# Kernel optimization log

Hardware: AMD Instinct MI355X
Metric: run time of the kernel (lower is better)

## Reference

```python
import jax, jax.numpy as jnp
import numpy as np

N_TOKEN = 267735
D = 512           # d_embed == d_proj
DIV = 4
CUTS = [0, 20000, 40000, 200000, 267735]  # cutoff_ends
N_TOKENS_BATCH = 1024  # len*bsz


def setup_inputs() -> dict:
    key = jax.random.key(0)
    ks = jax.random.split(key, 16)
    inp = {}
    inp["hidden"] = jax.random.normal(ks[0], (N_TOKENS_BATCH, D), jnp.float32)
    inp["target"] = jax.random.randint(ks[1], (N_TOKENS_BATCH,), 0, N_TOKEN)
    d_embs = [D // DIV ** i for i in range(4)]          # 512, 128, 32, 8
    sizes = [CUTS[i + 1] - CUTS[i] for i in range(4)]   # 20000, 20000, 160000, 67735
    for i in range(4):
        inp[f"W{i}"] = jax.random.normal(ks[2 + 3 * i], (sizes[i], d_embs[i]), jnp.float32) * (d_embs[i] ** -0.5)
        inp[f"b{i}"] = jax.random.normal(ks[3 + 3 * i], (sizes[i],), jnp.float32) * 0.01
        inp[f"proj{i}"] = jax.random.normal(ks[4 + 3 * i], (D, d_embs[i]), jnp.float32) * (D ** -0.5)
    inp["cluster_weight"] = jax.random.normal(ks[14], (3, D), jnp.float32) * (D ** -0.5)
    inp["cluster_bias"] = jax.random.normal(ks[15], (3,), jnp.float32) * 0.01
    return inp


def reference(hidden, target, W0, b0, proj0, W1, b1, proj1, W2, b2, proj2, W3, b3, proj3, cluster_weight, cluster_bias):
    n = jnp.arange(target.shape[0])
    # head = shortlist vocab + one logit per tail cluster
    head_w = jnp.concatenate([W0, cluster_weight], axis=0)   # [20003, D]
    head_b = jnp.concatenate([b0, cluster_bias], axis=0)     # [20003]
    head_logit = (hidden @ proj0) @ head_w.T + head_b        # einsum('bd,de,ev->bv')
    head_lp = jax.nn.log_softmax(head_logit, axis=-1)        # [N, 20003]
    head_size = head_lp.shape[1]
    # cluster id per token (0 = shortlist, 1..3 = tails)
    cid = ((target >= CUTS[1]).astype(jnp.int32)
           + (target >= CUTS[2]).astype(jnp.int32)
           + (target >= CUTS[3]).astype(jnp.int32))
    # shortlist: nll = -head_logprob[n, target]
    nll = -head_lp[n, jnp.clip(target, 0, CUTS[1] - 1)]
    for i, (Wi, bi, pi) in enumerate([(W1, b1, proj1), (W2, b2, proj2), (W3, b3, proj3)], start=1):
        l, r = CUTS[i], CUTS[i + 1]
        tail_lp = jax.nn.log_softmax((hidden @ pi) @ Wi.T + bi, axis=-1)  # [N, r-l]
        rel = jnp.clip(target - l, 0, r - l - 1)
        # faithful to original: head column indexed as head_logprob[:, -i]
        lp_i = head_lp[:, head_size - i] + tail_lp[n, rel]
        nll = jnp.where(cid == i, -lp_i, nll)
    return nll
```

## Files before the change

### kernel.cpp

```cpp
#include <hip/hip_runtime.h>

typedef short s16x8 __attribute__((ext_vector_type(8)));
typedef unsigned short u16x8 __attribute__((ext_vector_type(8)));
typedef float f32x4 __attribute__((ext_vector_type(4)));
typedef unsigned short ushort;

#define NTOK 1024
#define DHID 512

#define VH   20003
#define KH   512
#define NCH_H 80
#define TPC_H 16
#define VH_PAD 20480

#define V1   20000
#define K1   128
#define NCH_1 80
#define TPC_1 16
#define V1_PAD 20480

#define V2   160000
#define K2   32
#define NCH_2 128
#define TPC_2 80
#define V2_PAD 163840

#define V3   67735
#define K3   32
#define NCH_3 67
#define TPC_3 64
#define V3_PAD 68608

#define PAD_BIAS (-1e30f)

#define OFF_HW   0UL
#define OFF_W1   (OFF_HW  + (unsigned long)VH_PAD*KH*2)
#define OFF_W2   (OFF_W1  + (unsigned long)V1_PAD*K1*2)
#define OFF_W3   (OFF_W2  + (unsigned long)V2_PAD*K2*2)
#define OFF_HID  (OFF_W3  + (unsigned long)V3_PAD*K3*2)
#define OFF_PT0  (OFF_HID + (unsigned long)NTOK*DHID*2)
#define OFF_PT1  (OFF_PT0 + (unsigned long)512*DHID*2)
#define OFF_PT2  (OFF_PT1 + (unsigned long)128*DHID*2)
#define OFF_PT3  (OFF_PT2 + (unsigned long)32*DHID*2)
#define OFF_H0   (OFF_PT3 + (unsigned long)32*DHID*2)
#define OFF_H1   (OFF_H0  + (unsigned long)NTOK*512*2)
#define OFF_H2   (OFF_H1  + (unsigned long)NTOK*128*2)
#define OFF_H3   (OFF_H2  + (unsigned long)NTOK*32*2)
#define OFF_HB   (OFF_H3  + (unsigned long)NTOK*32*2)
#define OFF_B1   (OFF_HB  + (unsigned long)VH_PAD*4)
#define OFF_B2   (OFF_B1  + (unsigned long)V1_PAD*4)
#define OFF_B3   (OFF_B2  + (unsigned long)V2_PAD*4)
#define OFF_SH   (OFF_B3  + (unsigned long)V3_PAD*4)
#define OFF_S1   (OFF_SH  + (unsigned long)NTOK*NCH_H*4)
#define OFF_S2   (OFF_S1  + (unsigned long)NTOK*NCH_1*4)
#define OFF_S3   (OFF_S2  + (unsigned long)NTOK*NCH_2*4)

__device__ __forceinline__ ushort f2bf(float f) {
    union { float f; unsigned u; } x; x.f = f;
    unsigned r = x.u + 0x7fffu + ((x.u >> 16) & 1u);
    return (ushort)(r >> 16);
}
__device__ __forceinline__ float bf2f(ushort h) {
    union { unsigned u; float f; } x; x.u = ((unsigned)h) << 16;
    return x.f;
}
__device__ __forceinline__ f32x4 mfma_bf16(s16x8 a, s16x8 b, f32x4 c) {
    return __builtin_amdgcn_mfma_f32_16x16x32_bf16(a, b, c, 0, 0, 0);
}
__device__ __forceinline__ void ld8(const float* p, float* v) {
    float4 a = *(const float4*)p, b = *(const float4*)(p + 4);
    v[0]=a.x; v[1]=a.y; v[2]=a.z; v[3]=a.w; v[4]=b.x; v[5]=b.y; v[6]=b.z; v[7]=b.w;
}

#define WB_HW  20480L
#define WB_W1  5120L
#define WB_W2  10240L
#define WB_W3  4288L
#define WB_HID 1024L
#define WB_PT0 512L
#define WB_PT1 128L
#define WB_PT2 32L
#define WB_PT3 32L
#define WB_TOTAL (WB_HW+WB_W1+WB_W2+WB_W3+WB_HID+WB_PT0+WB_PT1+WB_PT2+WB_PT3)

__global__ __launch_bounds__(256) void prep_wswz(
    const float* __restrict__ hidden,
    const float* __restrict__ W0, const float* __restrict__ cw,
    const float* __restrict__ W1, const float* __restrict__ W2, const float* __restrict__ W3,
    const float* __restrict__ p0, const float* __restrict__ p1,
    const float* __restrict__ p2, const float* __restrict__ p3,
    ushort* __restrict__ hw, ushort* __restrict__ ow1,
    ushort* __restrict__ ow2, ushort* __restrict__ ow3,
    ushort* __restrict__ hid,
    ushort* __restrict__ pT0, ushort* __restrict__ pT1,
    ushort* __restrict__ pT2, ushort* __restrict__ pT3)
{
    int lane = threadIdx.x & 63;
    int r = lane & 15, quad = lane >> 4;
    long wb0 = (long)blockIdx.x * 4 + (threadIdx.x >> 6);
    long nw = (long)gridDim.x * 4;
    for (long wb = wb0; wb < WB_TOTAL; wb += nw) {
        long b = wb;
        float vals[8];
        #pragma unroll
        for (int j = 0; j < 8; ++j) vals[j] = 0.f;
        ushort* dst;
        if (b < WB_HW) {
            long tile = b >> 4, ks = b & 15;
            long v = tile * 16 + r, k = ks * 32 + quad * 8;
            if (v < 20000)      ld8(W0 + v * 512 + k, vals);
            else if (v < VH)    ld8(cw + (v - 20000) * 512 + k, vals);
            dst = hw + b * 512 + (long)lane * 8;
        } else if ((b -= WB_HW) < WB_W1) {
            long tile = b >> 2, ks = b & 3;
            long v = tile * 16 + r, k = ks * 32 + quad * 8;
            if (v < V1) ld8(W1 + v * 128 + k, vals);
            dst = ow1 + b * 512 + (long)lane * 8;
        } else if ((b -= WB_W1) < WB_W2) {
            long v = b * 16 + r;
            if (v < V2) ld8(W2 + v * 32 + quad * 8, vals);
            dst = ow2 + b * 512 + (long)lane * 8;
        } else if ((b -= WB_W2) < WB_W3) {
            long v = b * 16 + r;
            if (v < V3 && quad == 0) ld8(W3 + v * 8, vals);
            dst = ow3 + b * 512 + (long)lane * 8;
        } else if ((b -= WB_W3) < WB_HID) {
            long tile = b >> 4, ks = b & 15;
            long v = tile * 16 + r, k = ks * 32 + quad * 8;
            ld8(hidden + v * 512 + k, vals);
            dst = hid + b * 512 + (long)lane * 8;
        } else if ((b -= WB_HID) < WB_PT0) {
            long tile = b >> 4, ks = b & 15;
            long c = tile * 16 + r, k = ks * 32 + quad * 8;
            #pragma unroll
            for (int j = 0; j < 8; ++j) vals[j] = p0[(k + j) * 512 + c];
            dst = pT0 + b * 512 + (long)lane * 8;
        } else if ((b -= WB_PT0) < WB_PT1) {
            long tile = b >> 4, ks = b & 15;
            long c = tile * 16 + r, k = ks * 32 + quad * 8;
            #pragma unroll
            for (int j = 0; j < 8; ++j) vals[j] = p1[(k + j) * 128 + c];
            dst = pT1 + b * 512 + (long)lane * 8;
        } else if ((b -= WB_PT1) < WB_PT2) {
            long tile = b >> 4, ks = b & 15;
            long c = tile * 16 + r, k = ks * 32 + quad * 8;
            #pragma unroll
            for (int j = 0; j < 8; ++j) vals[j] = p2[(k + j) * 32 + c];
            dst = pT2 + b * 512 + (long)lane * 8;
        } else {
            b -= WB_PT2;
            long tile = b >> 4, ks = b & 15;
            long c = tile * 16 + r, k = ks * 32 + quad * 8;
            if (c < 8) {
                #pragma unroll
                for (int j = 0; j < 8; ++j) vals[j] = p3[(k + j) * 8 + c];
            }
            dst = pT3 + b * 512 + (long)lane * 8;
        }
        u16x8 o;
        #pragma unroll
        for (int j = 0; j < 8; ++j) o[j] = f2bf(vals[j]);
        *(u16x8*)dst = o;
    }
}

#define E_HB  ((long)VH_PAD)
#define E_B1  ((long)V1_PAD)
#define E_B2  ((long)V2_PAD)
#define E_B3  ((long)V3_PAD)
#define E_BIAS (E_HB+E_B1+E_B2+E_B3)

__global__ __launch_bounds__(256) void prep_bias(
    const float* __restrict__ b0, const float* __restrict__ b1,
    const float* __restrict__ b2, const float* __restrict__ b3,
    const float* __restrict__ cb,
    float* __restrict__ hbp, float* __restrict__ ob1,
    float* __restrict__ ob2, float* __restrict__ ob3)
{
    long stride = (long)gridDim.x * blockDim.x;
    for (long i = (long)blockIdx.x * blockDim.x + threadIdx.x; i < E_BIAS; i += stride) {
        long j = i;
        if (j < E_HB) {
            hbp[j] = (j < 20000) ? b0[j] : (j < VH) ? cb[j - 20000] : PAD_BIAS;
        } else if ((j -= E_HB) < E_B1) {
            ob1[j] = (j < V1) ? b1[j] : PAD_BIAS;
        } else if ((j -= E_B1) < E_B2) {
            ob2[j] = (j < V2) ? b2[j] : PAD_BIAS;
        } else { j -= E_B2;
            ob3[j] = (j < V3) ? b3[j] : PAD_BIAS;
        }
    }
}

__global__ __launch_bounds__(256) void gemm_h(
    const ushort* __restrict__ A, const ushort* __restrict__ Bt,
    ushort* __restrict__ Hout, int dpad)
{
    int wave = threadIdx.x >> 6, lane = threadIdx.x & 63;
    int quad = lane >> 4, colid = lane & 15;
    int m_tile = blockIdx.x * 4 + wave;
    int c_tile = blockIdx.y;
    const ushort* Ab = A + ((long)m_tile * 16) * 512 + lane * 8;
    const ushort* Bb = Bt + ((long)c_tile * 16) * 512 + lane * 8;
    f32x4 acc = {0.f, 0.f, 0.f, 0.f};
    #pragma unroll
    for (int ks = 0; ks < 16; ++ks) {
        s16x8 a = *(const s16x8*)(Ab + ks * 512);
        s16x8 b = *(const s16x8*)(Bb + ks * 512);
        acc = mfma_bf16(a, b, acc);
    }
    int KBo = dpad >> 5;
    int col = c_tile * 16 + colid;
    int ks_o = col >> 5, q_o = (col >> 3) & 3, j_o = col & 7;
    #pragma unroll
    for (int r = 0; r < 4; ++r) {
        int rm = quad * 4 + r;
        Hout[((long)m_tile * KBo + ks_o) * 512 + (q_o * 16 + rm) * 8 + j_o] = f2bf(acc[r]);
    }
}

template<int K, int U>
__global__ __launch_bounds__(256, 4) void fused_lse_t(
    const ushort* __restrict__ A, const ushort* __restrict__ W,
    const float* __restrict__ bias, float* __restrict__ part_s,
    int tpc, int n_chunks)
{
    constexpr int KB = K / 32;
    int wave = threadIdx.x >> 6, lane = threadIdx.x & 63;
    int quad = lane >> 4, colid = lane & 15;
    int m_tile = blockIdx.x * 4 + wave;
    int t0 = blockIdx.y * tpc;
    const ushort* Ab = A + ((long)m_tile * KB) * 512 + lane * 8;
    float s_acc[4] = {0.f, 0.f, 0.f, 0.f};

    for (int vt = 0; vt < tpc; vt += U) {
        int tile0 = t0 + vt;
        const ushort* Wb = W + ((long)tile0 * KB) * 512 + lane * 8;
        f32x4 acc[U];
        #pragma unroll
        for (int u = 0; u < U; ++u) acc[u] = (f32x4){0.f, 0.f, 0.f, 0.f};
        #pragma unroll 4
        for (int ks = 0; ks < KB; ++ks) {
            s16x8 a = *(const s16x8*)(Ab + ks * 512);
            #pragma unroll
            for (int u = 0; u < U; ++u) {
                s16x8 b = *(const s16x8*)(Wb + ((long)u * KB + ks) * 512);
                acc[u] = mfma_bf16(a, b, acc[u]);
            }
        }
        #pragma unroll
        for (int u = 0; u < U; ++u) {
            float bval = bias[(tile0 + u) * 16 + colid];
            #pragma unroll
            for (int r = 0; r < 4; ++r)
                s_acc[r] += __expf(acc[u][r] + bval);
        }
    }
    #pragma unroll
    for (int r = 0; r < 4; ++r) {
        float v = s_acc[r];
        v += __shfl_xor(v, 1);
        v += __shfl_xor(v, 2);
        v += __shfl_xor(v, 4);
        v += __shfl_xor(v, 8);
        s_acc[r] = v;
    }
    if (colid == 0) {
        #pragma unroll
        for (int r = 0; r < 4; ++r) {
            int m = m_tile * 16 + quad * 4 + r;
            part_s[(long)m * n_chunks + blockIdx.y] = s_acc[r];
        }
    }
}

__device__ __forceinline__ float swz_dot(const ushort* __restrict__ H, int m,
                                         const ushort* __restrict__ Wm, long vrow,
                                         int K, int lane)
{
    float d = 0.f;
    if (lane * 8 < K) {
        int ks = lane >> 2, q = lane & 3;
        int KB = K >> 5;
        const ushort* hp = H + ((long)(m >> 4) * KB + ks) * 512 + (q * 16 + (m & 15)) * 8;
        const ushort* wp = Wm + ((vrow >> 4) * KB + ks) * 512 + (q * 16 + (int)(vrow & 15)) * 8;
        #pragma unroll
        for (int j = 0; j < 8; ++j) d += bf2f(hp[j]) * bf2f(wp[j]);
    }
    d += __shfl_xor(d, 1);  d += __shfl_xor(d, 2);  d += __shfl_xor(d, 4);
    d += __shfl_xor(d, 8);  d += __shfl_xor(d, 16); d += __shfl_xor(d, 32);
    return d;
}

__global__ __launch_bounds__(256) void finalize_kernel(
    const int* __restrict__ target,
    const ushort* __restrict__ H0, const ushort* __restrict__ hw,
    const float* __restrict__ hbp, const float* __restrict__ sH,
    const ushort* __restrict__ H1, const ushort* __restrict__ w1,
    const float* __restrict__ b1p, const float* __restrict__ s1,
    const ushort* __restrict__ H2, const ushort* __restrict__ w2,
    const float* __restrict__ b2p, const float* __restrict__ s2,
    const ushort* __restrict__ H3, const ushort* __restrict__ w3,
    const float* __restrict__ b3p, const float* __restrict__ s3,
    float* __restrict__ out)
{
    int wave = threadIdx.x >> 6, lane = threadIdx.x & 63;
    int m = blockIdx.x * 4 + wave;
    int t = target[m];
    int cid = (t >= 20000) + (t >= 40000) + (t >= 200000);

    float s = 0.f;
    for (int i = lane; i < NCH_H; i += 64) s += sH[(long)m * NCH_H + i];
    s += __shfl_xor(s, 1);  s += __shfl_xor(s, 2);  s += __shfl_xor(s, 4);
    s += __shfl_xor(s, 8);  s += __shfl_xor(s, 16); s += __shfl_xor(s, 32);
    float lse_h = __logf(s);

    int hc = (cid == 0) ? t : (20003 - cid);
    float d = swz_dot(H0, m, hw, hc, 512, lane);
    float nll = lse_h - (d + hbp[hc]);

    if (cid > 0) {
        const ushort *Hi, *Wi; const float *bi, *si; int K, nc, l;
        if (cid == 1)      { Hi = H1; Wi = w1; bi = b1p; si = s1; K = 128; nc = NCH_1; l = 20000; }
        else if (cid == 2) { Hi = H2; Wi = w2; bi = b2p; si = s2; K = 32;  nc = NCH_2; l = 40000; }
        else               { Hi = H3; Wi = w3; bi = b3p; si = s3; K = 32;  nc = NCH_3; l = 200000; }
        int rel = t - l;
        float ts = 0.f;
        for (int i = lane; i < nc; i += 64) ts += si[(long)m * nc + i];
        ts += __shfl_xor(ts, 1);  ts += __shfl_xor(ts, 2);  ts += __shfl_xor(ts, 4);
        ts += __shfl_xor(ts, 8);  ts += __shfl_xor(ts, 16); ts += __shfl_xor(ts, 32);
        float lse_t = __logf(ts);
        float dt = swz_dot(Hi, m, Wi, rel, K, lane);
        nll += lse_t - (dt + bi[rel]);
    }
    if (lane == 0) out[m] = nll;
}

extern "C" void kernel_launch(void* const* d_in, const int* in_sizes, int n_in,
                              void* d_out, int out_size, void* d_ws, size_t ws_size,
                              hipStream_t stream) {
    const float* hidden = (const float*)d_in[0];
    const int*   target = (const int*)d_in[1];
    const float* W0 = (const float*)d_in[2];
    const float* b0 = (const float*)d_in[3];
    const float* p0 = (const float*)d_in[4];
    const float* W1 = (const float*)d_in[5];
    const float* b1 = (const float*)d_in[6];
    const float* p1 = (const float*)d_in[7];
    const float* W2 = (const float*)d_in[8];
    const float* b2 = (const float*)d_in[9];
    const float* p2 = (const float*)d_in[10];
    const float* W3 = (const float*)d_in[11];
    const float* b3 = (const float*)d_in[12];
    const float* p3 = (const float*)d_in[13];
    const float* cw = (const float*)d_in[14];
    const float* cb = (const float*)d_in[15];

    char* ws = (char*)d_ws;
    ushort* hw  = (ushort*)(ws + OFF_HW);
    ushort* ow1 = (ushort*)(ws + OFF_W1);
    ushort* ow2 = (ushort*)(ws + OFF_W2);
    ushort* ow3 = (ushort*)(ws + OFF_W3);
    ushort* hid = (ushort*)(ws + OFF_HID);
    ushort* pT0 = (ushort*)(ws + OFF_PT0);
    ushort* pT1 = (ushort*)(ws + OFF_PT1);
    ushort* pT2 = (ushort*)(ws + OFF_PT2);
    ushort* pT3 = (ushort*)(ws + OFF_PT3);
    ushort* H0  = (ushort*)(ws + OFF_H0);
    ushort* H1  = (ushort*)(ws + OFF_H1);
    ushort* H2  = (ushort*)(ws + OFF_H2);
    ushort* H3  = (ushort*)(ws + OFF_H3);
    float* hbp = (float*)(ws + OFF_HB);
    float* b1p = (float*)(ws + OFF_B1);
    float* b2p = (float*)(ws + OFF_B2);
    float* b3p = (float*)(ws + OFF_B3);
    float* sH  = (float*)(ws + OFF_SH);
    float* s1  = (float*)(ws + OFF_S1);
    float* s2  = (float*)(ws + OFF_S2);
    float* s3  = (float*)(ws + OFF_S3);

    prep_wswz<<<10464, 256, 0, stream>>>(hidden, W0, cw, W1, W2, W3,
                                         p0, p1, p2, p3,
                                         hw, ow1, ow2, ow3, hid, pT0, pT1, pT2, pT3);
    prep_bias<<<1072, 256, 0, stream>>>(b0, b1, b2, b3, cb, hbp, b1p, b2p, b3p);

    gemm_h<<<dim3(NTOK / 64, 512 / 16), 256, 0, stream>>>(hid, pT0, H0, 512);
    gemm_h<<<dim3(NTOK / 64, 128 / 16), 256, 0, stream>>>(hid, pT1, H1, 128);
    gemm_h<<<dim3(NTOK / 64, 32 / 16),  256, 0, stream>>>(hid, pT2, H2, 32);
    gemm_h<<<dim3(NTOK / 64, 32 / 16),  256, 0, stream>>>(hid, pT3, H3, 32);

    fused_lse_t<KH, 8><<<dim3(NTOK / 64, NCH_H), 256, 0, stream>>>(H0, hw,  hbp, sH, TPC_H, NCH_H);
    fused_lse_t<K1, 8><<<dim3(NTOK / 64, NCH_1), 256, 0, stream>>>(H1, ow1, b1p, s1, TPC_1, NCH_1);
    fused_lse_t<K2, 8><<<dim3(NTOK / 64, NCH_2), 256, 0, stream>>>(H2, ow2, b2p, s2, TPC_2, NCH_2);
    fused_lse_t<K3, 8><<<dim3(NTOK / 64, NCH_3), 256, 0, stream>>>(H3, ow3, b3p, s3, TPC_3, NCH_3);

    finalize_kernel<<<NTOK / 4, 256, 0, stream>>>(target,
        H0, hw, hbp, sH, H1, ow1, b1p, s1, H2, ow2, b2p, s2, H3, ow3, b3p, s3,
        (float*)d_out);
}
```

Baseline: 276.9 us.

## Stage vocab weight tiles through double-buffered LDS with async global-to-LDS loads

The fused log-sum-exp kernels now keep the A (hidden projection) fragments in registers for the whole block. Weight tiles are staged into two LDS buffers with global_load_lds, so all four waves share one copy instead of each reloading the same W tiles from global memory. The next group's load is meant to overlap with MFMA compute on the current group, and accumulation is split into two chains to shorten MFMA dependency chains. In exchange it adds barriers and vmcnt waits per group, raises register pressure for the head kernel (16 A fragments), and uses more LDS per block, which could limit occupancy.

```diff
diff --git a/kernel.cpp b/kernel.cpp
--- a/kernel.cpp
+++ b/kernel.cpp
@@ -73,6 +73,12 @@
     v[0]=a.x; v[1]=a.y; v[2]=a.z; v[3]=a.w; v[4]=b.x; v[5]=b.y; v[6]=b.z; v[7]=b.w;
 }
 
+__device__ __forceinline__ void gld_lds16(const ushort* g, ushort* l) {
+    __builtin_amdgcn_global_load_lds(
+        (const __attribute__((address_space(1))) unsigned int*)g,
+        (__attribute__((address_space(3))) unsigned int*)l, 16, 0, 0);
+}
+
 #define WB_HW  20480L
 #define WB_W1  5120L
 #define WB_W2  10240L
@@ -220,43 +226,99 @@
     }
 }
 
-template<int K, int U>
-__global__ __launch_bounds__(256, 4) void fused_lse_t(
+
+template<int TG>
+__device__ __forceinline__ void stage_grp(const ushort* __restrict__ gsrc_base,
+                                          ushort* __restrict__ buf,
+                                          int wave, int lane)
+{
+    constexpr int LPW = TG / 4;
+    const ushort* g = gsrc_base + ((long)wave * LPW) * 512 + lane * 8;
+    ushort* l = buf + (wave * LPW) * 512;
+    #pragma unroll
+    for (int i = 0; i < LPW; ++i)
+        gld_lds16(g + i * 512, l + i * 512);
+}
+
+template<int KB, int TG>
+__device__ __forceinline__ void compute_grp(const ushort* __restrict__ buf,
+                                            const s16x8 (&afrag)[KB],
+                                            const float* __restrict__ bias,
+                                            long tile0, int lane, int colid,
+                                            float (&s_acc)[4])
+{
+    constexpr int TPG = TG / KB;
+    f32x4 acc0[TPG], acc1[TPG];
+    #pragma unroll
+    for (int t = 0; t < TPG; ++t) {
+        acc0[t] = (f32x4){0.f, 0.f, 0.f, 0.f};
+        acc1[t] = (f32x4){0.f, 0.f, 0.f, 0.f};
+    }
+    #pragma unroll
+    for (int b = 0; b < TG; ++b) {
+        s16x8 bb = *(const s16x8*)(buf + b * 512 + lane * 8);
+        int t = b / KB, ks = b % KB;
+        if ((KB > 1) && (ks & 1))
+            acc1[t] = mfma_bf16(afrag[ks], bb, acc1[t]);
+        else
+            acc0[t] = mfma_bf16(afrag[ks], bb, acc0[t]);
+    }
+    #pragma unroll
+    for (int t = 0; t < TPG; ++t) {
+        float bval = bias[(tile0 + t) * 16 + colid];
+        #pragma unroll
+        for (int r = 0; r < 4; ++r) {
+            float v = acc0[t][r];
+            if (KB > 1) v += acc1[t][r];
+            s_acc[r] += __expf(v + bval);
+        }
+    }
+}
+
+template<int KB, int TG>
+__global__ __launch_bounds__(256, 4) void fused_lse_lds(
     const ushort* __restrict__ A, const ushort* __restrict__ W,
     const float* __restrict__ bias, float* __restrict__ part_s,
     int tpc, int n_chunks)
 {
-    constexpr int KB = K / 32;
+    constexpr int TPG = TG / KB;
+    __shared__ __align__(16) ushort lds0[TG * 512];
+    __shared__ __align__(16) ushort lds1[TG * 512];
+
     int wave = threadIdx.x >> 6, lane = threadIdx.x & 63;
     int quad = lane >> 4, colid = lane & 15;
     int m_tile = blockIdx.x * 4 + wave;
-    int t0 = blockIdx.y * tpc;
+    long t0 = (long)blockIdx.y * tpc;
+    const ushort* Wc = W + t0 * KB * 512;
+
+    s16x8 afrag[KB];
     const ushort* Ab = A + ((long)m_tile * KB) * 512 + lane * 8;
+    #pragma unroll
+    for (int ks = 0; ks < KB; ++ks) afrag[ks] = *(const s16x8*)(Ab + ks * 512);
+
+    const int ng = (tpc * KB) / TG;
     float s_acc[4] = {0.f, 0.f, 0.f, 0.f};
 
-    for (int vt = 0; vt < tpc; vt += U) {
-        int tile0 = t0 + vt;
-        const ushort* Wb = W + ((long)tile0 * KB) * 512 + lane * 8;
-        f32x4 acc[U];
-        #pragma unroll
-        for (int u = 0; u < U; ++u) acc[u] = (f32x4){0.f, 0.f, 0.f, 0.f};
-        #pragma unroll 4
-        for (int ks = 0; ks < KB; ++ks) {
-            s16x8 a = *(const s16x8*)(Ab + ks * 512);
-            #pragma unroll
-            for (int u = 0; u < U; ++u) {
-                s16x8 b = *(const s16x8*)(Wb + ((long)u * KB + ks) * 512);
-                acc[u] = mfma_bf16(a, b, acc[u]);
-            }
+    stage_grp<TG>(Wc, lds0, wave, lane);
+    asm volatile("s_waitcnt vmcnt(0)" ::: "memory");
+    __syncthreads();
+
+    for (int g = 0; g < ng; g += 2) {
+        if (g + 1 < ng)
+            stage_grp<TG>(Wc + ((long)(g + 1) * TG) * 512, lds1, wave, lane);
+        compute_grp<KB, TG>(lds0, afrag, bias, t0 + (long)g * TPG, lane, colid, s_acc);
+        asm volatile("s_waitcnt vmcnt(0)" ::: "memory");
+        __syncthreads();
+
+        if (g + 2 < ng)
+            stage_grp<TG>(Wc + ((long)(g + 2) * TG) * 512, lds0, wave, lane);
+        if (g + 1 < ng) {
+            compute_grp<KB, TG>(lds1, afrag, bias, t0 + (long)(g + 1) * TPG, lane, colid, s_acc);
+            asm volatile("s_waitcnt vmcnt(0)" ::: "memory");
+            __syncthreads();
         }
-        #pragma unroll
-        for (int u = 0; u < U; ++u) {
-            float bval = bias[(tile0 + u) * 16 + colid];
-            #pragma unroll
-            for (int r = 0; r < 4; ++r)
-                s_acc[r] += __expf(acc[u][r] + bval);
-        }
-    }
+    }
+
     #pragma unroll
     for (int r = 0; r < 4; ++r) {
         float v = s_acc[r];
@@ -390,10 +452,10 @@
     gemm_h<<<dim3(NTOK / 64, 32 / 16),  256, 0, stream>>>(hid, pT2, H2, 32);
     gemm_h<<<dim3(NTOK / 64, 32 / 16),  256, 0, stream>>>(hid, pT3, H3, 32);
 
-    fused_lse_t<KH, 8><<<dim3(NTOK / 64, NCH_H), 256, 0, stream>>>(H0, hw,  hbp, sH, TPC_H, NCH_H);
-    fused_lse_t<K1, 8><<<dim3(NTOK / 64, NCH_1), 256, 0, stream>>>(H1, ow1, b1p, s1, TPC_1, NCH_1);
-    fused_lse_t<K2, 8><<<dim3(NTOK / 64, NCH_2), 256, 0, stream>>>(H2, ow2, b2p, s2, TPC_2, NCH_2);
-    fused_lse_t<K3, 8><<<dim3(NTOK / 64, NCH_3), 256, 0, stream>>>(H3, ow3, b3p, s3, TPC_3, NCH_3);
+    fused_lse_lds<16, 16><<<dim3(NTOK / 64, NCH_H), 256, 0, stream>>>(H0, hw,  hbp, sH, TPC_H, NCH_H);
+    fused_lse_lds<4, 8><<<dim3(NTOK / 64, NCH_1), 256, 0, stream>>>(H1, ow1, b1p, s1, TPC_1, NCH_1);
+    fused_lse_lds<1, 8><<<dim3(NTOK / 64, NCH_2), 256, 0, stream>>>(H2, ow2, b2p, s2, TPC_2, NCH_2);
+    fused_lse_lds<1, 8><<<dim3(NTOK / 64, NCH_3), 256, 0, stream>>>(H3, ow3, b3p, s3, TPC_3, NCH_3);
 
     finalize_kernel<<<NTOK / 4, 256, 0, stream>>>(target,
         H0, hw, hbp, sH, H1, ow1, b1p, s1, H2, ow2, b2p, s2, H3, ow3, b3p, s3,
```

Result: faster. 261.9 us (-5.4%).

## Retile logsumexp GEMMs into 128x128 LDS-staged blocks with exp2 and merged projections

Applied to the files above, without the earlier changes.

Replaces the per-wave streaming LSE kernels with 128x128 block tiles: each wave computes a 4x4 grid of MFMA tiles fed through a triple-buffered LDS pipeline filled by direct global-to-LDS loads. K-loop and N-loop variants handle the wide and narrow-K clusters. Weights and biases are pre-scaled by log2(e) so the inner loop can use the native exp2, with the final dot product rescaled by ln2. The four projection GEMMs are merged into one launch. This raises operand reuse and cuts global traffic per MFMA, at the cost of more partial-sum chunks, more LDS per block, and a slight change in bf16 rounding from the pre-scaling.

```diff
diff --git a/kernel.cpp b/kernel.cpp
--- a/kernel.cpp
+++ b/kernel.cpp
@@ -10,29 +10,28 @@
 
 #define VH   20003
 #define KH   512
-#define NCH_H 80
-#define TPC_H 16
 #define VH_PAD 20480
 
 #define V1   20000
 #define K1   128
-#define NCH_1 80
-#define TPC_1 16
 #define V1_PAD 20480
 
 #define V2   160000
 #define K2   32
-#define NCH_2 128
-#define TPC_2 80
 #define V2_PAD 163840
 
 #define V3   67735
 #define K3   32
-#define NCH_3 67
-#define TPC_3 64
 #define V3_PAD 68608
 
+#define NCHK_H 320
+#define NCHK_1 320
+#define NCHK_2 320
+#define NCHK_3 134
+
 #define PAD_BIAS (-1e30f)
+#define LOG2E 1.4426950408889634f
+#define LN2F  0.6931471805599453f
 
 #define OFF_HW   0UL
 #define OFF_W1   (OFF_HW  + (unsigned long)VH_PAD*KH*2)
@@ -52,9 +51,9 @@
 #define OFF_B2   (OFF_B1  + (unsigned long)V1_PAD*4)
 #define OFF_B3   (OFF_B2  + (unsigned long)V2_PAD*4)
 #define OFF_SH   (OFF_B3  + (unsigned long)V3_PAD*4)
-#define OFF_S1   (OFF_SH  + (unsigned long)NTOK*NCH_H*4)
-#define OFF_S2   (OFF_S1  + (unsigned long)NTOK*NCH_1*4)
-#define OFF_S3   (OFF_S2  + (unsigned long)NTOK*NCH_2*4)
+#define OFF_S1   (OFF_SH  + (unsigned long)NTOK*NCHK_H*4)
+#define OFF_S2   (OFF_S1  + (unsigned long)NTOK*NCHK_1*4)
+#define OFF_S3   (OFF_S2  + (unsigned long)NTOK*NCHK_2*4)
 
 __device__ __forceinline__ ushort f2bf(float f) {
     union { float f; unsigned u; } x; x.f = f;
@@ -71,6 +70,11 @@
 __device__ __forceinline__ void ld8(const float* p, float* v) {
     float4 a = *(const float4*)p, b = *(const float4*)(p + 4);
     v[0]=a.x; v[1]=a.y; v[2]=a.z; v[3]=a.w; v[4]=b.x; v[5]=b.y; v[6]=b.z; v[7]=b.w;
+}
+__device__ __forceinline__ void gld_lds16(const ushort* g, ushort* l) {
+    __builtin_amdgcn_global_load_lds(
+        (const __attribute__((address_space(1))) unsigned int*)g,
+        (__attribute__((address_space(3))) unsigned int*)l, 16, 0, 0);
 }
 
 #define WB_HW  20480L
@@ -105,6 +109,7 @@
         float vals[8];
         #pragma unroll
         for (int j = 0; j < 8; ++j) vals[j] = 0.f;
+        float scale = LOG2E;
         ushort* dst;
         if (b < WB_HW) {
             long tile = b >> 4, ks = b & 15;
@@ -126,29 +131,34 @@
             if (v < V3 && quad == 0) ld8(W3 + v * 8, vals);
             dst = ow3 + b * 512 + (long)lane * 8;
         } else if ((b -= WB_W3) < WB_HID) {
+            scale = 1.f;
             long tile = b >> 4, ks = b & 15;
             long v = tile * 16 + r, k = ks * 32 + quad * 8;
             ld8(hidden + v * 512 + k, vals);
             dst = hid + b * 512 + (long)lane * 8;
         } else if ((b -= WB_HID) < WB_PT0) {
+            scale = 1.f;
             long tile = b >> 4, ks = b & 15;
             long c = tile * 16 + r, k = ks * 32 + quad * 8;
             #pragma unroll
             for (int j = 0; j < 8; ++j) vals[j] = p0[(k + j) * 512 + c];
             dst = pT0 + b * 512 + (long)lane * 8;
         } else if ((b -= WB_PT0) < WB_PT1) {
+            scale = 1.f;
             long tile = b >> 4, ks = b & 15;
             long c = tile * 16 + r, k = ks * 32 + quad * 8;
             #pragma unroll
             for (int j = 0; j < 8; ++j) vals[j] = p1[(k + j) * 128 + c];
             dst = pT1 + b * 512 + (long)lane * 8;
         } else if ((b -= WB_PT1) < WB_PT2) {
+            scale = 1.f;
             long tile = b >> 4, ks = b & 15;
             long c = tile * 16 + r, k = ks * 32 + quad * 8;
             #pragma unroll
             for (int j = 0; j < 8; ++j) vals[j] = p2[(k + j) * 32 + c];
             dst = pT2 + b * 512 + (long)lane * 8;
         } else {
+            scale = 1.f;
             b -= WB_PT2;
             long tile = b >> 4, ks = b & 15;
             long c = tile * 16 + r, k = ks * 32 + quad * 8;
@@ -160,7 +170,7 @@
         }
         u16x8 o;
         #pragma unroll
-        for (int j = 0; j < 8; ++j) o[j] = f2bf(vals[j]);
+        for (int j = 0; j < 8; ++j) o[j] = f2bf(vals[j] * scale);
         *(u16x8*)dst = o;
     }
 }
@@ -182,25 +192,24 @@
     for (long i = (long)blockIdx.x * blockDim.x + threadIdx.x; i < E_BIAS; i += stride) {
         long j = i;
         if (j < E_HB) {
-            hbp[j] = (j < 20000) ? b0[j] : (j < VH) ? cb[j - 20000] : PAD_BIAS;
+            hbp[j] = ((j < 20000) ? b0[j] : (j < VH) ? cb[j - 20000] : PAD_BIAS) * LOG2E;
         } else if ((j -= E_HB) < E_B1) {
-            ob1[j] = (j < V1) ? b1[j] : PAD_BIAS;
+            ob1[j] = ((j < V1) ? b1[j] : PAD_BIAS) * LOG2E;
         } else if ((j -= E_B1) < E_B2) {
-            ob2[j] = (j < V2) ? b2[j] : PAD_BIAS;
+            ob2[j] = ((j < V2) ? b2[j] : PAD_BIAS) * LOG2E;
         } else { j -= E_B2;
-            ob3[j] = (j < V3) ? b3[j] : PAD_BIAS;
+            ob3[j] = ((j < V3) ? b3[j] : PAD_BIAS) * LOG2E;
         }
     }
 }
 
-__global__ __launch_bounds__(256) void gemm_h(
+__device__ __forceinline__ void gemm_body(
     const ushort* __restrict__ A, const ushort* __restrict__ Bt,
-    ushort* __restrict__ Hout, int dpad)
+    ushort* __restrict__ Hout, int dpad, int c_tile)
 {
     int wave = threadIdx.x >> 6, lane = threadIdx.x & 63;
     int quad = lane >> 4, colid = lane & 15;
     int m_tile = blockIdx.x * 4 + wave;
-    int c_tile = blockIdx.y;
     const ushort* Ab = A + ((long)m_tile * 16) * 512 + lane * 8;
     const ushort* Bb = Bt + ((long)c_tile * 16) * 512 + lane * 8;
     f32x4 acc = {0.f, 0.f, 0.f, 0.f};
@@ -220,59 +229,221 @@
     }
 }
 
-template<int K, int U>
-__global__ __launch_bounds__(256, 4) void fused_lse_t(
+__global__ __launch_bounds__(256) void gemm_all(
+    const ushort* __restrict__ hid,
+    const ushort* __restrict__ pT0, const ushort* __restrict__ pT1,
+    const ushort* __restrict__ pT2, const ushort* __restrict__ pT3,
+    ushort* __restrict__ H0, ushort* __restrict__ H1,
+    ushort* __restrict__ H2, ushort* __restrict__ H3)
+{
+    int y = blockIdx.y;
+    if (y < 32)      gemm_body(hid, pT0, H0, 512, y);
+    else if (y < 40) gemm_body(hid, pT1, H1, 128, y - 32);
+    else if (y < 42) gemm_body(hid, pT2, H2, 32,  y - 40);
+    else             gemm_body(hid, pT3, H3, 32,  y - 42);
+}
+
+template<int KB>
+__global__ __launch_bounds__(256, 3) void gemm_lse_k(
     const ushort* __restrict__ A, const ushort* __restrict__ W,
-    const float* __restrict__ bias, float* __restrict__ part_s,
-    int tpc, int n_chunks)
-{
-    constexpr int KB = K / 32;
+    const float* __restrict__ biasp, float* __restrict__ part_s,
+    int n_chunks)
+{
+    __shared__ __align__(16) ushort lds[3 * 16 * 512];
+    int bid = blockIdx.x;
+    int k = bid & 7, j = bid >> 3;
+    int nb = k * 20 + (j >> 3);
+    int mb = j & 7;
     int wave = threadIdx.x >> 6, lane = threadIdx.x & 63;
+    int wr = wave >> 1, wc = wave & 1;
     int quad = lane >> 4, colid = lane & 15;
-    int m_tile = blockIdx.x * 4 + wave;
-    int t0 = blockIdx.y * tpc;
-    const ushort* Ab = A + ((long)m_tile * KB) * 512 + lane * 8;
-    float s_acc[4] = {0.f, 0.f, 0.f, 0.f};
-
-    for (int vt = 0; vt < tpc; vt += U) {
-        int tile0 = t0 + vt;
-        const ushort* Wb = W + ((long)tile0 * KB) * 512 + lane * 8;
-        f32x4 acc[U];
-        #pragma unroll
-        for (int u = 0; u < U; ++u) acc[u] = (f32x4){0.f, 0.f, 0.f, 0.f};
-        #pragma unroll 4
-        for (int ks = 0; ks < KB; ++ks) {
-            s16x8 a = *(const s16x8*)(Ab + ks * 512);
+
+    f32x4 acc[4][4];
+    #pragma unroll
+    for (int mi = 0; mi < 4; ++mi)
+        #pragma unroll
+        for (int ni = 0; ni < 4; ++ni) acc[mi][ni] = (f32x4){0.f, 0.f, 0.f, 0.f};
+
+    const long Abase = (long)mb * 8, Wbase = (long)nb * 8;
+
+#define STAGE_K(ks, bf) do {                                                     \
+        ushort* d_ = lds + (bf) * (16 * 512);                                    \
+        _Pragma("unroll")                                                        \
+        for (int i_ = 0; i_ < 2; ++i_) {                                         \
+            int t_ = 2 * wave + i_;                                              \
+            gld_lds16(A + ((Abase + t_) * KB + (ks)) * 512 + lane * 8,           \
+                      d_ + t_ * 512 + lane * 8);                                 \
+            gld_lds16(W + ((Wbase + t_) * KB + (ks)) * 512 + lane * 8,           \
+                      d_ + (8 + t_) * 512 + lane * 8);                           \
+        }                                                                        \
+    } while (0)
+
+#define COMP_K(bf) do {                                                          \
+        const ushort* b_ = lds + (bf) * (16 * 512);                              \
+        s16x8 af[4], bfg[4];                                                     \
+        _Pragma("unroll")                                                        \
+        for (int mi = 0; mi < 4; ++mi)                                           \
+            af[mi] = *(const s16x8*)(b_ + (wr * 4 + mi) * 512 + lane * 8);       \
+        _Pragma("unroll")                                                        \
+        for (int ni = 0; ni < 4; ++ni)                                           \
+            bfg[ni] = *(const s16x8*)(b_ + (8 + wc * 4 + ni) * 512 + lane * 8);  \
+        _Pragma("unroll")                                                        \
+        for (int mi = 0; mi < 4; ++mi)                                           \
+            _Pragma("unroll")                                                    \
+            for (int ni = 0; ni < 4; ++ni)                                       \
+                acc[mi][ni] = mfma_bf16(af[mi], bfg[ni], acc[mi][ni]);           \
+    } while (0)
+
+    STAGE_K(0, 0);
+    STAGE_K(1, 1);
+    for (int g = 0; g < KB - 1; ++g) {
+        asm volatile("s_waitcnt vmcnt(4)" ::: "memory");
+        __builtin_amdgcn_s_barrier();
+        if (g + 2 < KB) STAGE_K(g + 2, (g + 2) % 3);
+        COMP_K(g % 3);
+        asm volatile("s_waitcnt lgkmcnt(0)" ::: "memory");
+    }
+    asm volatile("s_waitcnt vmcnt(0)" ::: "memory");
+    __builtin_amdgcn_s_barrier();
+    COMP_K((KB - 1) % 3);
+#undef STAGE_K
+#undef COMP_K
+
+    float bv[4];
+    long c0 = (long)nb * 128 + wc * 64 + colid;
+    #pragma unroll
+    for (int ni = 0; ni < 4; ++ni) bv[ni] = biasp[c0 + ni * 16];
+    int chunk = nb * 2 + wc;
+    #pragma unroll
+    for (int mi = 0; mi < 4; ++mi) {
+        #pragma unroll
+        for (int r = 0; r < 4; ++r) {
+            float v = 0.f;
             #pragma unroll
-            for (int u = 0; u < U; ++u) {
-                s16x8 b = *(const s16x8*)(Wb + ((long)u * KB + ks) * 512);
-                acc[u] = mfma_bf16(a, b, acc[u]);
+            for (int ni = 0; ni < 4; ++ni)
+                v += __builtin_amdgcn_exp2f(acc[mi][ni][r] + bv[ni]);
+            v += __shfl_xor(v, 1);
+            v += __shfl_xor(v, 2);
+            v += __shfl_xor(v, 4);
+            v += __shfl_xor(v, 8);
+            if (colid == 0) {
+                int m = mb * 128 + wr * 64 + mi * 16 + quad * 4 + r;
+                part_s[(long)m * n_chunks + chunk] = v;
             }
         }
-        #pragma unroll
-        for (int u = 0; u < U; ++u) {
-            float bval = bias[(tile0 + u) * 16 + colid];
-            #pragma unroll
-            for (int r = 0; r < 4; ++r)
-                s_acc[r] += __expf(acc[u][r] + bval);
+    }
+}
+
+__global__ __launch_bounds__(256, 3) void gemm_lse_n(
+    const ushort* __restrict__ A, const ushort* __restrict__ W,
+    const float* __restrict__ biasp, float* __restrict__ part_s,
+    int n_chunks, int vng, int ngmax)
+{
+    __shared__ __align__(16) ushort ldsA[8 * 512];
+    __shared__ __align__(16) ushort ldsW[3 * 8 * 512];
+    __shared__ float ldsB[1024];
+    int bid = blockIdx.x;
+    int k = bid & 7, j = bid >> 3;
+    int ng = k * vng + (j >> 3);
+    int mb = j & 7;
+    if (ng >= ngmax) return;
+    int wave = threadIdx.x >> 6, lane = threadIdx.x & 63;
+    int wr = wave >> 1, wc = wave & 1;
+    int quad = lane >> 4, colid = lane & 15;
+
+    #pragma unroll
+    for (int i = 0; i < 2; ++i) {
+        int t = 2 * wave + i;
+        gld_lds16(A + ((long)(mb * 8 + t)) * 512 + lane * 8, ldsA + t * 512 + lane * 8);
+    }
+    for (int i = threadIdx.x; i < 1024; i += 256) ldsB[i] = biasp[(long)ng * 1024 + i];
+    __syncthreads();
+
+    s16x8 af[4];
+    #pragma unroll
+    for (int mi = 0; mi < 4; ++mi)
+        af[mi] = *(const s16x8*)(ldsA + (wr * 4 + mi) * 512 + lane * 8);
+
+    float s_acc[4][4];
+    #pragma unroll
+    for (int mi = 0; mi < 4; ++mi)
+        #pragma unroll
+        for (int r = 0; r < 4; ++r) s_acc[mi][r] = 0.f;
+
+    const long Wg = (long)ng * 64;
+
+#define STAGE_N(t, bf) do {                                                      \
+        ushort* d_ = ldsW + (bf) * (8 * 512);                                    \
+        _Pragma("unroll")                                                        \
+        for (int i_ = 0; i_ < 2; ++i_) {                                         \
+            int b_ = 2 * wave + i_;                                              \
+            gld_lds16(W + (Wg + (t) * 8 + b_) * 512 + lane * 8,                  \
+                      d_ + b_ * 512 + lane * 8);                                 \
+        }                                                                        \
+    } while (0)
+
+#define COMP_N(t, bf) do {                                                       \
+        const ushort* wb_ = ldsW + (bf) * (8 * 512);                             \
+        s16x8 bfg[4];                                                            \
+        float bv_[4];                                                            \
+        _Pragma("unroll")                                                        \
+        for (int ni = 0; ni < 4; ++ni) {                                         \
+            bfg[ni] = *(const s16x8*)(wb_ + (wc * 4 + ni) * 512 + lane * 8);     \
+            bv_[ni] = ldsB[(t) * 128 + wc * 64 + ni * 16 + colid];               \
+        }                                                                        \
+        f32x4 acc_[4][4];                                                        \
+        _Pragma("unroll")                                                        \
+        for (int mi = 0; mi < 4; ++mi)                                           \
+            _Pragma("unroll")                                                    \
+            for (int ni = 0; ni < 4; ++ni)                                       \
+                acc_[mi][ni] = (f32x4){bv_[ni], bv_[ni], bv_[ni], bv_[ni]};      \
+        _Pragma("unroll")                                                        \
+        for (int mi = 0; mi < 4; ++mi)                                           \
+            _Pragma("unroll")                                                    \
+            for (int ni = 0; ni < 4; ++ni)                                       \
+                acc_[mi][ni] = mfma_bf16(af[mi], bfg[ni], acc_[mi][ni]);         \
+        _Pragma("unroll")                                                        \
+        for (int mi = 0; mi < 4; ++mi)                                           \
+            _Pragma("unroll")                                                    \
+            for (int r = 0; r < 4; ++r) {                                        \
+                float v_ = 0.f;                                                  \
+                _Pragma("unroll")                                                \
+                for (int ni = 0; ni < 4; ++ni)                                   \
+                    v_ += __builtin_amdgcn_exp2f(acc_[mi][ni][r]);               \
+                s_acc[mi][r] += v_;                                              \
+            }                                                                    \
+    } while (0)
+
+    STAGE_N(0, 0);
+    STAGE_N(1, 1);
+    for (int t = 0; t < 7; ++t) {
+        asm volatile("s_waitcnt vmcnt(2)" ::: "memory");
+        __builtin_amdgcn_s_barrier();
+        if (t + 2 < 8) STAGE_N(t + 2, (t + 2) % 3);
+        COMP_N(t, t % 3);
+        asm volatile("s_waitcnt lgkmcnt(0)" ::: "memory");
+    }
+    asm volatile("s_waitcnt vmcnt(0)" ::: "memory");
+    __builtin_amdgcn_s_barrier();
+    COMP_N(7, 7 % 3);
+#undef STAGE_N
+#undef COMP_N
+
+    int chunk = ng * 2 + wc;
+    #pragma unroll
+    for (int mi = 0; mi < 4; ++mi)
+        #pragma unroll
+        for (int r = 0; r < 4; ++r) {
+            float v = s_acc[mi][r];
+            v += __shfl_xor(v, 1);
+            v += __shfl_xor(v, 2);
+            v += __shfl_xor(v, 4);
+            v += __shfl_xor(v, 8);
+            if (colid == 0) {
+                int m = mb * 128 + wr * 64 + mi * 16 + quad * 4 + r;
+                part_s[(long)m * n_chunks + chunk] = v;
+            }
         }
-    }
-    #pragma unroll
-    for (int r = 0; r < 4; ++r) {
-        float v = s_acc[r];
-        v += __shfl_xor(v, 1);
-        v += __shfl_xor(v, 2);
-        v += __shfl_xor(v, 4);
-        v += __shfl_xor(v, 8);
-        s_acc[r] = v;
-    }
-    if (colid == 0) {
-        #pragma unroll
-        for (int r = 0; r < 4; ++r) {
-            int m = m_tile * 16 + quad * 4 + r;
-            part_s[(long)m * n_chunks + blockIdx.y] = s_acc[r];
-        }
-    }
 }
 
 __device__ __forceinline__ float swz_dot(const ushort* __restrict__ H, int m,
@@ -311,20 +482,20 @@
     int cid = (t >= 20000) + (t >= 40000) + (t >= 200000);
 
     float s = 0.f;
-    for (int i = lane; i < NCH_H; i += 64) s += sH[(long)m * NCH_H + i];
+    for (int i = lane; i < NCHK_H; i += 64) s += sH[(long)m * NCHK_H + i];
     s += __shfl_xor(s, 1);  s += __shfl_xor(s, 2);  s += __shfl_xor(s, 4);
     s += __shfl_xor(s, 8);  s += __shfl_xor(s, 16); s += __shfl_xor(s, 32);
     float lse_h = __logf(s);
 
     int hc = (cid == 0) ? t : (20003 - cid);
     float d = swz_dot(H0, m, hw, hc, 512, lane);
-    float nll = lse_h - (d + hbp[hc]);
+    float nll = lse_h - (d + hbp[hc]) * LN2F;
 
     if (cid > 0) {
         const ushort *Hi, *Wi; const float *bi, *si; int K, nc, l;
-        if (cid == 1)      { Hi = H1; Wi = w1; bi = b1p; si = s1; K = 128; nc = NCH_1; l = 20000; }
-        else if (cid == 2) { Hi = H2; Wi = w2; bi = b2p; si = s2; K = 32;  nc = NCH_2; l = 40000; }
-        else               { Hi = H3; Wi = w3; bi = b3p; si = s3; K = 32;  nc = NCH_3; l = 200000; }
+        if (cid == 1)      { Hi = H1; Wi = w1; bi = b1p; si = s1; K = 128; nc = NCHK_1; l = 20000; }
+        else if (cid == 2) { Hi = H2; Wi = w2; bi = b2p; si = s2; K = 32;  nc = NCHK_2; l = 40000; }
+        else               { Hi = H3; Wi = w3; bi = b3p; si = s3; K = 32;  nc = NCHK_3; l = 200000; }
         int rel = t - l;
         float ts = 0.f;
         for (int i = lane; i < nc; i += 64) ts += si[(long)m * nc + i];
@@ -332,7 +503,7 @@
         ts += __shfl_xor(ts, 8);  ts += __shfl_xor(ts, 16); ts += __shfl_xor(ts, 32);
         float lse_t = __logf(ts);
         float dt = swz_dot(Hi, m, Wi, rel, K, lane);
-        nll += lse_t - (dt + bi[rel]);
+        nll += lse_t - (dt + bi[rel]) * LN2F;
     }
     if (lane == 0) out[m] = nll;
 }
@@ -385,15 +556,13 @@
                                          hw, ow1, ow2, ow3, hid, pT0, pT1, pT2, pT3);
     prep_bias<<<1072, 256, 0, stream>>>(b0, b1, b2, b3, cb, hbp, b1p, b2p, b3p);
 
-    gemm_h<<<dim3(NTOK / 64, 512 / 16), 256, 0, stream>>>(hid, pT0, H0, 512);
-    gemm_h<<<dim3(NTOK / 64, 128 / 16), 256, 0, stream>>>(hid, pT1, H1, 128);
-    gemm_h<<<dim3(NTOK / 64, 32 / 16),  256, 0, stream>>>(hid, pT2, H2, 32);
-    gemm_h<<<dim3(NTOK / 64, 32 / 16),  256, 0, stream>>>(hid, pT3, H3, 32);
-
-    fused_lse_t<KH, 8><<<dim3(NTOK / 64, NCH_H), 256, 0, stream>>>(H0, hw,  hbp, sH, TPC_H, NCH_H);
-    fused_lse_t<K1, 8><<<dim3(NTOK / 64, NCH_1), 256, 0, stream>>>(H1, ow1, b1p, s1, TPC_1, NCH_1);
-    fused_lse_t<K2, 8><<<dim3(NTOK / 64, NCH_2), 256, 0, stream>>>(H2, ow2, b2p, s2, TPC_2, NCH_2);
-    fused_lse_t<K3, 8><<<dim3(NTOK / 64, NCH_3), 256, 0, stream>>>(H3, ow3, b3p, s3, TPC_3, NCH_3);
+    gemm_all<<<dim3(NTOK / 64, 44), 256, 0, stream>>>(hid, pT0, pT1, pT2, pT3,
+                                                      H0, H1, H2, H3);
+
+    gemm_lse_k<16><<<1280, 256, 0, stream>>>(H0, hw, hbp, sH, NCHK_H);
+    gemm_lse_k<4><<<1280, 256, 0, stream>>>(H1, ow1, b1p, s1, NCHK_1);
+    gemm_lse_n<<<1280, 256, 0, stream>>>(H2, ow2, b2p, s2, NCHK_2, 20, 160);
+    gemm_lse_n<<<576, 256, 0, stream>>>(H3, ow3, b3p, s3, NCHK_3, 9, 67);
 
     finalize_kernel<<<NTOK / 4, 256, 0, stream>>>(target,
         H0, hw, hbp, sH, H1, ow1, b1p, s1, H2, ow2, b2p, s2, H3, ow3, b3p, s3,
```

Result: slower. 534.9 us (+93.2%).
